# Kernel tuning notes

Measured on AMD Instinct MI355X. Metric: run time of the kernel, lower is better.

Reference implementation:

```python
import jax, jax.numpy as jnp
import numpy as np

EPS = 1e-5
KH = KW = 3
PAD = 1

def conv3x3(x, w, b=None):
    out = jax.lax.conv_general_dilated(
        x, w, window_strides=(1, 1), padding=((PAD, PAD), (PAD, PAD)),
        dimension_numbers=("NCHW", "OIHW", "NCHW"))
    if b is not None:
        out = out + b[None, :, None, None]
    return out

def batchnorm(x, gamma, beta):
    # training-mode BatchNorm2d: batch statistics over (N, H, W)
    mean = x.mean(axis=(0, 2, 3), keepdims=True)
    var = x.var(axis=(0, 2, 3), keepdims=True)
    return gamma[None, :, None, None] * (x - mean) / jnp.sqrt(var + EPS) + beta[None, :, None, None]

def bilinear_gather(x, y_pos, x_pos):
    # x: [B,C,H,W]; y_pos/x_pos: [B,P,H,W] (P = KH*KW sampling taps)
    # zero padding outside image (mmcv modulated deform conv semantics)
    B, C, H, W = x.shape
    P = y_pos.shape[1]
    x_flat = x.reshape(B, C, H * W)
    y0 = jnp.floor(y_pos)
    x0 = jnp.floor(x_pos)
    ly = y_pos - y0
    lx = x_pos - x0
    out = jnp.zeros((B, C, P, H, W), dtype=x.dtype)
    for dy, dx, wgt in ((0, 0, (1 - ly) * (1 - lx)), (0, 1, (1 - ly) * lx),
                        (1, 0, ly * (1 - lx)), (1, 1, ly * lx)):
        yi = y0 + dy
        xi = x0 + dx
        valid = ((yi >= 0) & (yi <= H - 1) & (xi >= 0) & (xi <= W - 1)).astype(x.dtype)
        yc = jnp.clip(yi, 0, H - 1).astype(jnp.int32)
        xc = jnp.clip(xi, 0, W - 1).astype(jnp.int32)
        idx = (yc * W + xc).reshape(B, 1, P * H * W)
        vals = jnp.take_along_axis(x_flat, jnp.broadcast_to(idx, (B, C, P * H * W)), axis=2)
        vals = vals.reshape(B, C, P, H, W)
        out = out + vals * (wgt * valid)[:, None]
    return out  # [B,C,P,H,W]

def modulated_deform_conv(x, w_off, b_off, w_dcn):
    B, C, H, W = x.shape
    P = KH * KW
    off = conv3x3(x, w_off, b_off)  # [B, 3*P, H, W]
    o1, o2, m = jnp.split(off, 3, axis=1)
    offset = jnp.concatenate([o1, o2], axis=1)            # [B, 2P, H, W]
    offset = offset.reshape(B, P, 2, H, W)                # channel 2p -> dy, 2p+1 -> dx
    mask = jax.nn.sigmoid(m)                              # [B, P, H, W]
    hh = jnp.arange(H, dtype=x.dtype)
    ww = jnp.arange(W, dtype=x.dtype)
    ky = jnp.arange(KH, dtype=x.dtype)
    kx = jnp.arange(KW, dtype=x.dtype)
    # base sampling grid per tap p = ky*KW + kx: (h - PAD + ky, w - PAD + kx)
    base_y = (hh[None, :] - PAD + ky[:, None])            # [KH, H]
    base_x = (ww[None, :] - PAD + kx[:, None])            # [KW, W]
    base_y = jnp.broadcast_to(base_y[:, None, :, None], (KH, KW, H, W)).reshape(P, H, W)
    base_x = jnp.broadcast_to(base_x[None, :, None, :], (KH, KW, H, W)).reshape(P, H, W)
    y_pos = base_y[None] + offset[:, :, 0]                # [B,P,H,W]
    x_pos = base_x[None] + offset[:, :, 1]
    sampled = bilinear_gather(x, y_pos, x_pos)            # [B,C,P,H,W]
    sampled = sampled * mask[:, None]
    w = w_dcn.reshape(w_dcn.shape[0], C, P)               # [O, C, P]
    return jnp.einsum("bcphw,ocp->bohw", sampled, w)

def setup_inputs() -> dict:
    key = jax.random.key(0)
    ks = jax.random.split(key, 10)
    B, Ch, H, W = 4, 256, 64, 64
    Cin, Cout = 2 * Ch, 256
    P = KH * KW
    inp = {
        "input_v": jax.random.normal(ks[0], (B, Ch, H, W), jnp.float32),
        "input_i": jax.random.normal(ks[1], (B, Ch, H, W), jnp.float32),
        "w_off": jax.random.normal(ks[2], (3 * P, Cin, KH, KW), jnp.float32) * 0.01,
        "b_off": jnp.zeros((3 * P,), jnp.float32),
        "w_dcn": jax.random.normal(ks[3], (Cout, Cin, KH, KW), jnp.float32) * (1.0 / np.sqrt(Cin * P)),
        "gamma1": jnp.ones((Cout,), jnp.float32),
        "beta1": jnp.zeros((Cout,), jnp.float32),
        "w2": jax.random.normal(ks[4], (Cout, Cout, KH, KW), jnp.float32) * (1.0 / np.sqrt(Cout * P)),
        "gamma2": jnp.ones((Cout,), jnp.float32),
        "beta2": jnp.zeros((Cout,), jnp.float32),
    }
    return inp

def reference(input_v, input_i, w_off, b_off, w_dcn, gamma1, beta1, w2, gamma2, beta2):
    x = jnp.concatenate([input_v, input_i], axis=1)
    out = modulated_deform_conv(x, w_off, b_off, w_dcn)
    out = jax.nn.relu(batchnorm(out, gamma1, beta1))
    out = jax.nn.relu(batchnorm(conv3x3(out, w2), gamma2, beta2))
    return out
```

## Files before the change

kernel.cpp:

```cpp
#include <hip/hip_runtime.h>
#include <cstdint>
#include <cstddef>

typedef unsigned short u16;
typedef __attribute__((ext_vector_type(8))) short s16x8;
typedef __attribute__((ext_vector_type(4))) float f32x4;

#define DEV __device__ __forceinline__

DEV float bf2f(short u){
  union { unsigned int i; float f; } v;
  v.i = ((unsigned int)(u16)u) << 16;
  return v.f;
}
DEV short f2bf(float f){
  union { float f; unsigned int i; } v; v.f = f;
  unsigned int u = v.i;
  u += 0x7fffu + ((u >> 16) & 1u);
  return (short)(u >> 16);
}
DEV s16x8 s16x8_zero(){
  s16x8 z;
#pragma unroll
  for(int j=0;j<8;j++) z[j]=0;
  return z;
}
DEV f32x4 f32x4_zero(){
  f32x4 z;
#pragma unroll
  for(int j=0;j<4;j++) z[j]=0.f;
  return z;
}
DEV f32x4 mfma16(s16x8 a, s16x8 b, f32x4 c){
  return __builtin_amdgcn_mfma_f32_16x16x32_bf16(a, b, c, 0, 0, 0);
}
DEV void bar_lds(){
  asm volatile("s_waitcnt lgkmcnt(0)");
  __builtin_amdgcn_s_barrier();
}
DEV void gload16(const u16* g, u16* l){
  __builtin_amdgcn_global_load_lds(
      (const __attribute__((address_space(1))) unsigned int*)g,
      (__attribute__((address_space(3))) unsigned int*)l, 16, 0, 0);
}

static constexpr size_t OFF_ACC_B   = 0;
static constexpr size_t STATS_B     = 2097152;
static constexpr size_t OUT1_ACC_B  = 2101248;
static constexpr size_t OUT2_ACC_B  = 18878464;
static constexpr size_t XN_PAD_B    = 35655680;
static constexpr size_t OUT1N_PAD_B = 53497856;
static constexpr size_t ZERO_BYTES  = 62418944;
static constexpr size_t S_B         = 62418944;
static constexpr size_t WOFFT_B     = 213708800;
static constexpr size_t WDCNT_B     = 214003712;
static constexpr size_t W2T_B       = 216363008;
static constexpr size_t POFS_B      = 217542656;
static constexpr size_t PWGT_B      = 219901952;

__global__ void k_x_to_nhwc(const float* __restrict__ v, const float* __restrict__ vi,
                            u16* __restrict__ xn){
  __shared__ float tile[64][65];
  const int b = blockIdx.z, c0 = blockIdx.y*64, hw0 = blockIdx.x*64;
  const int h = hw0 >> 6;
  const float* src = (c0 < 256) ? (v  + ((size_t)b*256 + c0)      *4096)
                                : (vi + ((size_t)b*256 + (c0-256))*4096);
  const int t = threadIdx.x;
#pragma unroll
  for(int k=0;k<16;k++){
    int idx = t + k*256;
    int cl = idx >> 6, wl = idx & 63;
    tile[cl][wl] = src[(size_t)cl*4096 + hw0 + wl];
  }
  __syncthreads();
#pragma unroll
  for(int k=0;k<16;k++){
    int idx = t + k*256;
    int wl = idx >> 6, cl = idx & 63;
    xn[((size_t)(b*66 + h+1)*66 + wl+1)*512 + c0 + cl] = (u16)f2bf(tile[cl][wl]);
  }
}

__global__ void k_prep_woff(const float* __restrict__ w, u16* __restrict__ wt){
  int idx = blockIdx.x*256 + threadIdx.x;
  if(idx >= 32*4608) return;
  int n = idx / 4608, k = idx % 4608;
  int t = k >> 9, c = k & 511;
  float val = (n < 27) ? w[(size_t)(n*512 + c)*9 + t] : 0.f;
  wt[idx] = (u16)f2bf(val);
}
__global__ void k_prep_wdcn(const float* __restrict__ w, u16* __restrict__ wt){
  int idx = blockIdx.x*256 + threadIdx.x;
  if(idx >= 256*4608) return;
  int n = idx / 4608, k = idx % 4608;
  int t = k >> 9, c = k & 511;
  wt[idx] = (u16)f2bf(w[(size_t)(n*512 + c)*9 + t]);
}
__global__ void k_prep_w2(const float* __restrict__ w, u16* __restrict__ wt){
  int idx = blockIdx.x*256 + threadIdx.x;
  if(idx >= 256*2304) return;
  int n = idx / 2304, k = idx % 2304;
  int t = k >> 8, c = k & 255;
  wt[idx] = (u16)f2bf(w[(size_t)(n*256 + c)*9 + t]);
}

__global__ __launch_bounds__(256, 2) void k_conv_off(
    const u16* __restrict__ xn, const u16* __restrict__ wt, float* __restrict__ offa){
  __shared__ short A_lds[4][128][8];
  __shared__ short B_lds[4][32][8];
  const int tid = threadIdx.x;
  const int lane = tid & 63, wid = tid >> 6;
  const int quad = lane >> 4, ln = lane & 15;
  const int m0 = blockIdx.x * 128;
  const int b = m0 >> 12;
  const int h0 = (m0 & 4095) >> 6;
  const int ks = blockIdx.y;
  const int ts0 = (ks == 3) ? 6 : ks*2;
  const int ntap = (ks == 3) ? 3 : 2;
  const int m_base = wid * 32;
  const int r = tid >> 1, sp = (tid & 1) * 2;
  const int h_r = h0 + (r >> 6), w_r = r & 63;
  const s16x8* Ap = (const s16x8*)A_lds;
  const s16x8* Bp = (const s16x8*)B_lds;
  f32x4 acc[2][2];
#pragma unroll
  for(int mf=0;mf<2;mf++)
#pragma unroll
    for(int nf=0;nf<2;nf++) acc[mf][nf] = f32x4_zero();

  auto load_it = [&](int it, s16x8& v0, s16x8& v1, s16x8& bv){
    const int tp = ts0 + (it >> 4);
    const int cA = (it & 15)*32;
    const int ty = tp/3, tx = tp - ty*3;
    const int y = h_r + ty, x = w_r + tx;
    const u16* src = xn + ((size_t)(b*66 + y)*66 + x)*512 + cA + sp*8;
    v0 = *(const s16x8*)(src);
    v1 = *(const s16x8*)(src + 8);
    if(tid < 128){
      const int n = tid & 31, s2 = tid >> 5;
      bv = *(const s16x8*)(wt + (size_t)n*4608 + tp*512 + cA + s2*8);
    }
  };

  const int NIT = ntap * 16;
  s16x8 v0a, v1a, bva, v0b, v1b, bvb;
  bva = s16x8_zero(); bvb = s16x8_zero();
  load_it(0, v0a, v1a, bva);
  load_it(1, v0b, v1b, bvb);
  for(int it = 0; it < NIT; it += 2){
    bar_lds();
    *(s16x8*)(&A_lds[sp][r][0])   = v0a;
    *(s16x8*)(&A_lds[sp+1][r][0]) = v1a;
    if(tid < 128){
      const int n = tid & 31, s2 = tid >> 5;
      *(s16x8*)(&B_lds[s2][n][0]) = bva;
    }
    if(it + 2 < NIT) load_it(it + 2, v0a, v1a, bva);
    bar_lds();
    {
      s16x8 a0 = Ap[quad*128 + m_base + ln];
      s16x8 a1 = Ap[quad*128 + m_base + 16 + ln];
      s16x8 b0 = Bp[quad*32 + ln];
      s16x8 b1 = Bp[quad*32 + 16 + ln];
      acc[0][0] = mfma16(a0, b0, acc[0][0]);
      acc[0][1] = mfma16(a0, b1, acc[0][1]);
      acc[1][0] = mfma16(a1, b0, acc[1][0]);
      acc[1][1] = mfma16(a1, b1, acc[1][1]);
    }
    bar_lds();
    *(s16x8*)(&A_lds[sp][r][0])   = v0b;
    *(s16x8*)(&A_lds[sp+1][r][0]) = v1b;
    if(tid < 128){
      const int n = tid & 31, s2 = tid >> 5;
      *(s16x8*)(&B_lds[s2][n][0]) = bvb;
    }
    if(it + 3 < NIT) load_it(it + 3, v0b, v1b, bvb);
    bar_lds();
    {
      s16x8 a0 = Ap[quad*128 + m_base + ln];
      s16x8 a1 = Ap[quad*128 + m_base + 16 + ln];
      s16x8 b0 = Bp[quad*32 + ln];
      s16x8 b1 = Bp[quad*32 + 16 + ln];
      acc[0][0] = mfma16(a0, b0, acc[0][0]);
      acc[0][1] = mfma16(a0, b1, acc[0][1]);
      acc[1][0] = mfma16(a1, b0, acc[1][0]);
      acc[1][1] = mfma16(a1, b1, acc[1][1]);
    }
  }
#pragma unroll
  for(int mf=0;mf<2;mf++)
#pragma unroll
    for(int nf=0;nf<2;nf++){
      const int col = nf*16 + ln;
#pragma unroll
      for(int i=0;i<4;i++){
        const int row = m_base + mf*16 + quad*4 + i;
        unsafeAtomicAdd(offa + (size_t)(m0+row)*32 + col, acc[mf][nf][i]);
      }
    }
}

__global__ void k_prep_off2(const float* __restrict__ offa, const float* __restrict__ boff,
                            int* __restrict__ pofs, float* __restrict__ pwgt){
  int id = blockIdx.x*256 + threadIdx.x;
  if(id >= 16384*9) return;
  int m = id / 9, tp = id - m*9;
  int b = m >> 12, h = (m >> 6) & 63, w = m & 63;
  const float* orow = offa + (size_t)m*32;
  float dy = orow[2*tp]   + boff[2*tp];
  float dx = orow[2*tp+1] + boff[2*tp+1];
  float mz = orow[18+tp]  + boff[18+tp];
  float mk = 1.f / (1.f + expf(-mz));
  float ypos = (float)(h - 1 + tp/3) + dy;
  float xpos = (float)(w - 1 + tp%3) + dx;
  float y0f = floorf(ypos), x0f = floorf(xpos);
  float ly = ypos - y0f, lx = xpos - x0f;
  int y0 = (int)y0f, x0 = (int)x0f;
#pragma unroll
  for(int k=0;k<4;k++){
    int ddy = k >> 1, ddx = k & 1;
    int yi = y0 + ddy, xi = x0 + ddx;
    int yc = yi < -1 ? -1 : (yi > 64 ? 64 : yi);
    int xc = xi < -1 ? -1 : (xi > 64 ? 64 : xi);
    float wk = (ddy ? ly : 1.f-ly) * (ddx ? lx : 1.f-lx) * mk;
    pofs[id*4+k] = ((b*66 + yc+1)*66 + xc+1) << 9;
    pwgt[id*4+k] = wk;
  }
}

__global__ __launch_bounds__(256) void k_sample(
    const u16* __restrict__ xn, const int* __restrict__ pofs,
    const float* __restrict__ pwgt, u16* __restrict__ S){
  const int wid = threadIdx.x >> 6, lane = threadIdx.x & 63;
  const int m = blockIdx.x*4 + wid;
  const int tp = blockIdx.y;
  const int id4 = (m*9 + tp)*4;
  const int4   of = *(const int4*)  (pofs + id4);
  const float4 wg = *(const float4*)(pwgt + id4);
  const int c0 = lane*8;
  s16x8 g0 = *(const s16x8*)(xn + of.x + c0);
  s16x8 g1 = *(const s16x8*)(xn + of.y + c0);
  s16x8 g2 = *(const s16x8*)(xn + of.z + c0);
  s16x8 g3 = *(const s16x8*)(xn + of.w + c0);
  s16x8 pk;
#pragma unroll
  for(int j=0;j<8;j++){
    float f = wg.x * bf2f(g0[j]);
    f = fmaf(wg.y, bf2f(g1[j]), f);
    f = fmaf(wg.z, bf2f(g2[j]), f);
    f = fmaf(wg.w, bf2f(g3[j]), f);
    pk[j] = f2bf(f);
  }
  *(s16x8*)(S + (size_t)m*4608 + tp*512 + c0) = pk;
}

__global__ __launch_bounds__(256, 4) void k_gemm1(
    const u16* __restrict__ S, const u16* __restrict__ wt, float* __restrict__ outa){
  __shared__ short A_lds[8][64][8];
  __shared__ short B_lds[8][128][8];
  const int tid = threadIdx.x;
  const int lane = tid & 63, wid = tid >> 6;
  const int quad = lane >> 4, ln = lane & 15;
  const int wm = wid >> 1, wn = wid & 1;
  const int m0 = blockIdx.x * 64;
  const int n0 = blockIdx.y * 128;
  const int kbase = blockIdx.z * 2304;
  const u16* Arow = S + (size_t)(m0 + lane)*4608;
  f32x4 acc[2][4];
#pragma unroll
  for(int mf=0;mf<2;mf++)
#pragma unroll
    for(int nf=0;nf<4;nf++) acc[mf][nf] = f32x4_zero();

  for(int t = 0; t < 36; ++t){
    const int k0 = kbase + t*64;
#pragma unroll
    for(int i=0;i<2;i++){
      const int g = wid*2 + i;
      gload16(Arow + k0 + g*8, (u16*)&A_lds[g][0][0]);
    }
#pragma unroll
    for(int i=0;i<4;i++){
      const int g2 = wid*4 + i;
      gload16(wt + (size_t)(n0 + (g2&1)*64 + lane)*4608 + k0 + (g2>>1)*8,
              (u16*)&B_lds[g2>>1][(g2&1)*64][0]);
    }
    __syncthreads();
#pragma unroll
    for(int kk=0;kk<2;kk++){
      s16x8 af[2], bf[4];
#pragma unroll
      for(int mf=0;mf<2;mf++)
        af[mf] = *(const s16x8*)&A_lds[kk*4+quad][wm*32 + mf*16 + ln][0];
#pragma unroll
      for(int nf=0;nf<4;nf++)
        bf[nf] = *(const s16x8*)&B_lds[kk*4+quad][wn*64 + nf*16 + ln][0];
#pragma unroll
      for(int mf=0;mf<2;mf++)
#pragma unroll
        for(int nf=0;nf<4;nf++)
          acc[mf][nf] = mfma16(af[mf], bf[nf], acc[mf][nf]);
    }
    __syncthreads();
  }
#pragma unroll
  for(int mf=0;mf<2;mf++)
#pragma unroll
    for(int nf=0;nf<4;nf++){
      const int col = n0 + wn*64 + nf*16 + ln;
#pragma unroll
      for(int i=0;i<4;i++){
        const int row = m0 + wm*32 + mf*16 + quad*4 + i;
        unsafeAtomicAdd(outa + (size_t)row*256 + col, acc[mf][nf][i]);
      }
    }
}

__global__ __launch_bounds__(256, 4) void k_gemm2(
    const u16* __restrict__ a_pad, const u16* __restrict__ wt, float* __restrict__ outa){
  __shared__ short A_lds[8][64][8];
  __shared__ short B_lds[8][128][8];
  const int tid = threadIdx.x;
  const int lane = tid & 63, wid = tid >> 6;
  const int quad = lane >> 4, ln = lane & 15;
  const int wm = wid >> 1, wn = wid & 1;
  const int m0 = blockIdx.x * 64;
  const int n0 = blockIdx.y * 128;
  const int kbase = blockIdx.z * 1152;
  const int b = m0 >> 12;
  const int h = (m0 & 4095) >> 6;
  f32x4 acc[2][4];
#pragma unroll
  for(int mf=0;mf<2;mf++)
#pragma unroll
    for(int nf=0;nf<4;nf++) acc[mf][nf] = f32x4_zero();

  for(int t = 0; t < 18; ++t){
    const int k0 = kbase + t*64;
    const int tp = k0 >> 8, cit = k0 & 255;
    const int ty = tp/3, tx = tp - ty*3;
    const u16* Arow = a_pad + ((size_t)(b*66 + h + ty)*66 + lane + tx)*256 + cit;
#pragma unroll
    for(int i=0;i<2;i++){
      const int g = wid*2 + i;
      gload16(Arow + g*8, (u16*)&A_lds[g][0][0]);
    }
#pragma unroll
    for(int i=0;i<4;i++){
      const int g2 = wid*4 + i;
      gload16(wt + (size_t)(n0 + (g2&1)*64 + lane)*2304 + k0 + (g2>>1)*8,
              (u16*)&B_lds[g2>>1][(g2&1)*64][0]);
    }
    __syncthreads();
#pragma unroll
    for(int kk=0;kk<2;kk++){
      s16x8 af[2], bf[4];
#pragma unroll
      for(int mf=0;mf<2;mf++)
        af[mf] = *(const s16x8*)&A_lds[kk*4+quad][wm*32 + mf*16 + ln][0];
#pragma unroll
      for(int nf=0;nf<4;nf++)
        bf[nf] = *(const s16x8*)&B_lds[kk*4+quad][wn*64 + nf*16 + ln][0];
#pragma unroll
      for(int mf=0;mf<2;mf++)
#pragma unroll
        for(int nf=0;nf<4;nf++)
          acc[mf][nf] = mfma16(af[mf], bf[nf], acc[mf][nf]);
    }
    __syncthreads();
  }
#pragma unroll
  for(int mf=0;mf<2;mf++)
#pragma unroll
    for(int nf=0;nf<4;nf++){
      const int col = n0 + wn*64 + nf*16 + ln;
#pragma unroll
      for(int i=0;i<4;i++){
        const int row = m0 + wm*32 + mf*16 + quad*4 + i;
        unsafeAtomicAdd(outa + (size_t)row*256 + col, acc[mf][nf][i]);
      }
    }
}

__global__ void k_stats(const float* __restrict__ acc, float* __restrict__ sum,
                        float* __restrict__ sq){
  const int m0 = blockIdx.x*64;
  const int c = threadIdx.x;
  float s = 0.f, q = 0.f;
  for(int i=0;i<64;i++){
    float v = acc[(size_t)(m0+i)*256 + c];
    s += v; q += v*v;
  }
  unsafeAtomicAdd(sum + c, s);
  unsafeAtomicAdd(sq + c, q);
}

__global__ void k_bn1(const float* __restrict__ acc, const float* __restrict__ sum,
                      const float* __restrict__ sq, const float* __restrict__ g,
                      const float* __restrict__ bt, u16* __restrict__ o){
  __shared__ float sc[256], sh[256];
  const int t = threadIdx.x;
  {
    float mean = sum[t] * (1.f/16384.f);
    float var  = sq[t] * (1.f/16384.f) - mean*mean;
    float rstd = rsqrtf(var + 1e-5f);
    float s = g[t] * rstd;
    sc[t] = s; sh[t] = bt[t] - mean*s;
  }
  __syncthreads();
  const int c4 = (t & 63) * 4;
  const float s0 = sc[c4], s1 = sc[c4+1], s2 = sc[c4+2], s3 = sc[c4+3];
  const float h0 = sh[c4], h1 = sh[c4+1], h2 = sh[c4+2], h3 = sh[c4+3];
#pragma unroll
  for(int k=0;k<4;k++){
    int m = blockIdx.x*16 + k*4 + (t>>6);
    int b = m >> 12, hh = (m >> 6) & 63, ww = m & 63;
    const float4 v = *(const float4*)(acc + (size_t)m*256 + c4);
    unsigned int lo = (unsigned int)(u16)f2bf(fmaxf(0.f, v.x*s0 + h0))
                    | ((unsigned int)(u16)f2bf(fmaxf(0.f, v.y*s1 + h1)) << 16);
    unsigned int hi = (unsigned int)(u16)f2bf(fmaxf(0.f, v.z*s2 + h2))
                    | ((unsigned int)(u16)f2bf(fmaxf(0.f, v.w*s3 + h3)) << 16);
    uint2 pr; pr.x = lo; pr.y = hi;
    *(uint2*)(o + ((size_t)(b*66 + hh+1)*66 + ww+1)*256 + c4) = pr;
  }
}

__global__ void k_bn2_out(const float* __restrict__ acc, const float* __restrict__ sum,
                          const float* __restrict__ sq, const float* __restrict__ g,
                          const float* __restrict__ bt, float* __restrict__ out){
  __shared__ float tile[64][65];
  __shared__ float sc[64], sh[64];
  const int t = threadIdx.x;
  const int b = blockIdx.z, c0 = blockIdx.y*64, hw0 = blockIdx.x*64;
  if(t < 64){
    int c = c0 + t;
    float mean = sum[c] * (1.f/16384.f);
    float var  = sq[c] * (1.f/16384.f) - mean*mean;
    float rstd = rsqrtf(var + 1e-5f);
    float s = g[c] * rstd;
    sc[t] = s; sh[t] = bt[c] - mean*s;
  }
  __syncthreads();
#pragma unroll
  for(int k=0;k<16;k++){
    int idx = t + k*256;
    int wl = idx >> 6, cl = idx & 63;
    float v = acc[(size_t)((b<<12) + hw0 + wl)*256 + c0 + cl];
    tile[wl][cl] = fmaxf(0.f, v*sc[cl] + sh[cl]);
  }
  __syncthreads();
#pragma unroll
  for(int k=0;k<16;k++){
    int idx = t + k*256;
    int cl = idx >> 6, wl = idx & 63;
    out[(size_t)(b*256 + c0 + cl)*4096 + hw0 + wl] = tile[wl][cl];
  }
}

extern "C" void kernel_launch(void* const* d_in, const int* in_sizes, int n_in,
                              void* d_out, int out_size, void* d_ws, size_t ws_size,
                              hipStream_t stream){
  const float* in_v  = (const float*)d_in[0];
  const float* in_i  = (const float*)d_in[1];
  const float* w_off = (const float*)d_in[2];
  const float* b_off = (const float*)d_in[3];
  const float* w_dcn = (const float*)d_in[4];
  const float* g1    = (const float*)d_in[5];
  const float* bt1   = (const float*)d_in[6];
  const float* w2    = (const float*)d_in[7];
  const float* g2    = (const float*)d_in[8];
  const float* bt2   = (const float*)d_in[9];
  float* out = (float*)d_out;
  char* ws = (char*)d_ws;

  float* off_acc   = (float*)(ws + OFF_ACC_B);
  float* stats     = (float*)(ws + STATS_B);
  float* out1_acc  = (float*)(ws + OUT1_ACC_B);
  float* out2_acc  = (float*)(ws + OUT2_ACC_B);
  u16*   xn_pad    = (u16*)  (ws + XN_PAD_B);
  u16*   out1n_pad = (u16*)  (ws + OUT1N_PAD_B);
  u16*   Smat      = (u16*)  (ws + S_B);
  u16*   wofft     = (u16*)  (ws + WOFFT_B);
  u16*   wdcnt     = (u16*)  (ws + WDCNT_B);
  u16*   w2t       = (u16*)  (ws + W2T_B);
  int*   pofs      = (int*)  (ws + POFS_B);
  float* pwgt      = (float*)(ws + PWGT_B);
  float* sum1 = stats,       *sq1 = stats + 256;
  float* sum2 = stats + 512, *sq2 = stats + 768;

  hipMemsetAsync(ws, 0, ZERO_BYTES, stream);
  k_x_to_nhwc<<<dim3(64,8,4), 256, 0, stream>>>(in_v, in_i, xn_pad);
  k_prep_woff<<<576, 256, 0, stream>>>(w_off, wofft);
  k_prep_wdcn<<<4608, 256, 0, stream>>>(w_dcn, wdcnt);
  k_prep_w2<<<2304, 256, 0, stream>>>(w2, w2t);
  k_conv_off<<<dim3(128,4), 256, 0, stream>>>(xn_pad, wofft, off_acc);
  k_prep_off2<<<576, 256, 0, stream>>>(off_acc, b_off, pofs, pwgt);
  k_sample<<<dim3(4096,9), 256, 0, stream>>>(xn_pad, pofs, pwgt, Smat);
  k_gemm1<<<dim3(256,2,2), 256, 0, stream>>>(Smat, wdcnt, out1_acc);
  k_stats<<<256, 256, 0, stream>>>(out1_acc, sum1, sq1);
  k_bn1<<<1024, 256, 0, stream>>>(out1_acc, sum1, sq1, g1, bt1, out1n_pad);
  k_gemm2<<<dim3(256,2,2), 256, 0, stream>>>(out1n_pad, w2t, out2_acc);
  k_stats<<<256, 256, 0, stream>>>(out2_acc, sum2, sq2);
  k_bn2_out<<<dim3(64,4,4), 256, 0, stream>>>(out2_acc, sum2, sq2, g2, bt2, out);
}
```

Measured before the change: 428.3 us.

## Double-buffer LDS and enlarge M tile to 128 in both GEMM kernels

Both implicit GEMMs now use 128x128 block tiles instead of 64x128, with twice the accumulators per wave, and double-buffered LDS stages. The global loads for stage t+2 are issued while stage t is computed, and waits use partial vmcnt. This is meant to hide load latency and raise MFMA reuse per loaded byte, at the cost of fewer blocks (512 per GEMM), more registers and LDS, and lower occupancy.

```diff
diff --git a/kernel.cpp b/kernel.cpp
--- a/kernel.cpp
+++ b/kernel.cpp
@@ -254,129 +254,162 @@
   *(s16x8*)(S + (size_t)m*4608 + tp*512 + c0) = pk;
 }
 
-__global__ __launch_bounds__(256, 4) void k_gemm1(
+__global__ __launch_bounds__(256, 2) void k_gemm1(
     const u16* __restrict__ S, const u16* __restrict__ wt, float* __restrict__ outa){
-  __shared__ short A_lds[8][64][8];
-  __shared__ short B_lds[8][128][8];
+  __shared__ short A_lds[2][8][128][8];
+  __shared__ short B_lds[2][8][128][8];
   const int tid = threadIdx.x;
   const int lane = tid & 63, wid = tid >> 6;
   const int quad = lane >> 4, ln = lane & 15;
   const int wm = wid >> 1, wn = wid & 1;
-  const int m0 = blockIdx.x * 64;
+  const int m0 = blockIdx.x * 128;
   const int n0 = blockIdx.y * 128;
   const int kbase = blockIdx.z * 2304;
-  const u16* Arow = S + (size_t)(m0 + lane)*4608;
-  f32x4 acc[2][4];
-#pragma unroll
-  for(int mf=0;mf<2;mf++)
+  constexpr int NPH = 36;
+  f32x4 acc[4][4];
+#pragma unroll
+  for(int mf=0;mf<4;mf++)
 #pragma unroll
     for(int nf=0;nf<4;nf++) acc[mf][nf] = f32x4_zero();
 
-  for(int t = 0; t < 36; ++t){
+  auto stage = [&](int t, int bi){
     const int k0 = kbase + t*64;
 #pragma unroll
-    for(int i=0;i<2;i++){
-      const int g = wid*2 + i;
-      gload16(Arow + k0 + g*8, (u16*)&A_lds[g][0][0]);
-    }
-#pragma unroll
     for(int i=0;i<4;i++){
-      const int g2 = wid*4 + i;
-      gload16(wt + (size_t)(n0 + (g2&1)*64 + lane)*4608 + k0 + (g2>>1)*8,
-              (u16*)&B_lds[g2>>1][(g2&1)*64][0]);
-    }
-    __syncthreads();
+      const int idx = wid*4 + i;
+      const int s = idx >> 1, rh = (idx & 1)*64;
+      gload16(S  + (size_t)(m0 + rh + lane)*4608 + k0 + s*8, (u16*)&A_lds[bi][s][rh][0]);
+      gload16(wt + (size_t)(n0 + rh + lane)*4608 + k0 + s*8, (u16*)&B_lds[bi][s][rh][0]);
+    }
+  };
+  auto compute = [&](int bi){
 #pragma unroll
     for(int kk=0;kk<2;kk++){
-      s16x8 af[2], bf[4];
-#pragma unroll
-      for(int mf=0;mf<2;mf++)
-        af[mf] = *(const s16x8*)&A_lds[kk*4+quad][wm*32 + mf*16 + ln][0];
+      s16x8 af[4], bf[4];
+#pragma unroll
+      for(int mf=0;mf<4;mf++)
+        af[mf] = *(const s16x8*)&A_lds[bi][kk*4+quad][wm*64 + mf*16 + ln][0];
 #pragma unroll
       for(int nf=0;nf<4;nf++)
-        bf[nf] = *(const s16x8*)&B_lds[kk*4+quad][wn*64 + nf*16 + ln][0];
-#pragma unroll
-      for(int mf=0;mf<2;mf++)
+        bf[nf] = *(const s16x8*)&B_lds[bi][kk*4+quad][wn*64 + nf*16 + ln][0];
+#pragma unroll
+      for(int mf=0;mf<4;mf++)
 #pragma unroll
         for(int nf=0;nf<4;nf++)
           acc[mf][nf] = mfma16(af[mf], bf[nf], acc[mf][nf]);
     }
-    __syncthreads();
-  }
-#pragma unroll
-  for(int mf=0;mf<2;mf++)
+  };
+
+  stage(0, 0);
+  asm volatile("s_waitcnt vmcnt(0)");
+  __builtin_amdgcn_s_barrier();
+  stage(1, 1);
+  for(int t = 0; t < NPH; ++t){
+    const int bi = t & 1;
+    compute(bi);
+    bar_lds();
+    if(t + 2 < NPH){
+      stage(t + 2, bi);
+      asm volatile("s_waitcnt vmcnt(8)");
+    } else {
+      asm volatile("s_waitcnt vmcnt(0)");
+    }
+    __builtin_amdgcn_sched_barrier(0);
+    __builtin_amdgcn_s_barrier();
+  }
+
+#pragma unroll
+  for(int mf=0;mf<4;mf++)
 #pragma unroll
     for(int nf=0;nf<4;nf++){
       const int col = n0 + wn*64 + nf*16 + ln;
 #pragma unroll
       for(int i=0;i<4;i++){
-        const int row = m0 + wm*32 + mf*16 + quad*4 + i;
+        const int row = m0 + wm*64 + mf*16 + quad*4 + i;
         unsafeAtomicAdd(outa + (size_t)row*256 + col, acc[mf][nf][i]);
       }
     }
 }
 
-__global__ __launch_bounds__(256, 4) void k_gemm2(
+__global__ __launch_bounds__(256, 2) void k_gemm2(
     const u16* __restrict__ a_pad, const u16* __restrict__ wt, float* __restrict__ outa){
-  __shared__ short A_lds[8][64][8];
-  __shared__ short B_lds[8][128][8];
+  __shared__ short A_lds[2][8][128][8];
+  __shared__ short B_lds[2][8][128][8];
   const int tid = threadIdx.x;
   const int lane = tid & 63, wid = tid >> 6;
   const int quad = lane >> 4, ln = lane & 15;
   const int wm = wid >> 1, wn = wid & 1;
-  const int m0 = blockIdx.x * 64;
+  const int m0 = blockIdx.x * 128;
   const int n0 = blockIdx.y * 128;
   const int kbase = blockIdx.z * 1152;
   const int b = m0 >> 12;
-  const int h = (m0 & 4095) >> 6;
-  f32x4 acc[2][4];
-#pragma unroll
-  for(int mf=0;mf<2;mf++)
+  const int h0 = (m0 & 4095) >> 6;
+  constexpr int NPH = 18;
+  f32x4 acc[4][4];
+#pragma unroll
+  for(int mf=0;mf<4;mf++)
 #pragma unroll
     for(int nf=0;nf<4;nf++) acc[mf][nf] = f32x4_zero();
 
-  for(int t = 0; t < 18; ++t){
+  auto stage = [&](int t, int bi){
     const int k0 = kbase + t*64;
     const int tp = k0 >> 8, cit = k0 & 255;
     const int ty = tp/3, tx = tp - ty*3;
-    const u16* Arow = a_pad + ((size_t)(b*66 + h + ty)*66 + lane + tx)*256 + cit;
-#pragma unroll
-    for(int i=0;i<2;i++){
-      const int g = wid*2 + i;
-      gload16(Arow + g*8, (u16*)&A_lds[g][0][0]);
-    }
 #pragma unroll
     for(int i=0;i<4;i++){
-      const int g2 = wid*4 + i;
-      gload16(wt + (size_t)(n0 + (g2&1)*64 + lane)*2304 + k0 + (g2>>1)*8,
-              (u16*)&B_lds[g2>>1][(g2&1)*64][0]);
-    }
-    __syncthreads();
+      const int idx = wid*4 + i;
+      const int s = idx >> 1, rh = (idx & 1)*64;
+      const int hh = h0 + (rh >> 6) + ty;
+      gload16(a_pad + ((size_t)(b*66 + hh)*66 + lane + tx)*256 + cit + s*8,
+              (u16*)&A_lds[bi][s][rh][0]);
+      gload16(wt + (size_t)(n0 + rh + lane)*2304 + k0 + s*8,
+              (u16*)&B_lds[bi][s][rh][0]);
+    }
+  };
+  auto compute = [&](int bi){
 #pragma unroll
     for(int kk=0;kk<2;kk++){
-      s16x8 af[2], bf[4];
-#pragma unroll
-      for(int mf=0;mf<2;mf++)
-        af[mf] = *(const s16x8*)&A_lds[kk*4+quad][wm*32 + mf*16 + ln][0];
+      s16x8 af[4], bf[4];
+#pragma unroll
+      for(int mf=0;mf<4;mf++)
+        af[mf] = *(const s16x8*)&A_lds[bi][kk*4+quad][wm*64 + mf*16 + ln][0];
 #pragma unroll
       for(int nf=0;nf<4;nf++)
-        bf[nf] = *(const s16x8*)&B_lds[kk*4+quad][wn*64 + nf*16 + ln][0];
-#pragma unroll
-      for(int mf=0;mf<2;mf++)
+        bf[nf] = *(const s16x8*)&B_lds[bi][kk*4+quad][wn*64 + nf*16 + ln][0];
+#pragma unroll
+      for(int mf=0;mf<4;mf++)
 #pragma unroll
         for(int nf=0;nf<4;nf++)
           acc[mf][nf] = mfma16(af[mf], bf[nf], acc[mf][nf]);
     }
-    __syncthreads();
-  }
-#pragma unroll
-  for(int mf=0;mf<2;mf++)
+  };
+
+  stage(0, 0);
+  asm volatile("s_waitcnt vmcnt(0)");
+  __builtin_amdgcn_s_barrier();
+  stage(1, 1);
+  for(int t = 0; t < NPH; ++t){
+    const int bi = t & 1;
+    compute(bi);
+    bar_lds();
+    if(t + 2 < NPH){
+      stage(t + 2, bi);
+      asm volatile("s_waitcnt vmcnt(8)");
+    } else {
+      asm volatile("s_waitcnt vmcnt(0)");
+    }
+    __builtin_amdgcn_sched_barrier(0);
+    __builtin_amdgcn_s_barrier();
+  }
+
+#pragma unroll
+  for(int mf=0;mf<4;mf++)
 #pragma unroll
     for(int nf=0;nf<4;nf++){
       const int col = n0 + wn*64 + nf*16 + ln;
 #pragma unroll
       for(int i=0;i<4;i++){
-        const int row = m0 + wm*32 + mf*16 + quad*4 + i;
+        const int row = m0 + wm*64 + mf*16 + quad*4 + i;
         unsafeAtomicAdd(outa + (size_t)row*256 + col, acc[mf][nf][i]);
       }
     }
@@ -496,10 +529,10 @@
   k_conv_off<<<dim3(128,4), 256, 0, stream>>>(xn_pad, wofft, off_acc);
   k_prep_off2<<<576, 256, 0, stream>>>(off_acc, b_off, pofs, pwgt);
   k_sample<<<dim3(4096,9), 256, 0, stream>>>(xn_pad, pofs, pwgt, Smat);
-  k_gemm1<<<dim3(256,2,2), 256, 0, stream>>>(Smat, wdcnt, out1_acc);
+  k_gemm1<<<dim3(128,2,2), 256, 0, stream>>>(Smat, wdcnt, out1_acc);
   k_stats<<<256, 256, 0, stream>>>(out1_acc, sum1, sq1);
   k_bn1<<<1024, 256, 0, stream>>>(out1_acc, sum1, sq1, g1, bt1, out1n_pad);
-  k_gemm2<<<dim3(256,2,2), 256, 0, stream>>>(out1n_pad, w2t, out2_acc);
+  k_gemm2<<<dim3(128,2,2), 256, 0, stream>>>(out1n_pad, w2t, out2_acc);
   k_stats<<<256, 256, 0, stream>>>(out2_acc, sum2, sq2);
   k_bn2_out<<<dim3(64,4,4), 256, 0, stream>>>(out2_acc, sum2, sq2, g2, bt2, out);
 }
```

Result: faster. 392.5 us (-8.4%).
